# Kernel optimization log

Hardware: AMD Instinct MI355X
Metric: run time of the kernel (lower is better)

Reference implementation:

```python
import jax, jax.numpy as jnp
import numpy as np

EPS = 1e-06
H = 25  # num heads


def _rmsnorm(x, w, eps=EPS):
    # normalize over last dim in float32, as in the torch module
    xf = x.astype(jnp.float32)
    var = jnp.mean(xf * xf, axis=-1, keepdims=True)
    return (w * (xf * jax.lax.rsqrt(var + eps))).astype(x.dtype)


def setup_inputs() -> dict:
    key = jax.random.key(0)
    ks = jax.random.split(key, 4)
    B, N, C = 8, 1025, 3200
    x = jax.random.normal(ks[0], (B, N, C), dtype=jnp.float32)
    qkv_w = jax.random.normal(ks[1], (C, 3 * C), dtype=jnp.float32) * (C ** -0.5)
    qkv_b = jnp.zeros((3 * C,), dtype=jnp.float32)
    q_norm_w = jnp.ones((C,), dtype=jnp.float32)
    k_norm_w = jnp.ones((C,), dtype=jnp.float32)
    proj_w = jax.random.normal(ks[2], (C, C), dtype=jnp.float32) * (C ** -0.5)
    proj_b = jnp.zeros((C,), dtype=jnp.float32)
    return {"x": x, "qkv_w": qkv_w, "qkv_b": qkv_b, "q_norm_w": q_norm_w,
            "k_norm_w": k_norm_w, "proj_w": proj_w, "proj_b": proj_b}


def reference(x, qkv_w, qkv_b, q_norm_w, k_norm_w, proj_w, proj_b):
    B, N, C = x.shape
    D = C // H
    scale = D ** -0.5
    qkv = x @ qkv_w + qkv_b                      # [B, N, 3C]
    q, k, v = jnp.split(qkv, 3, axis=-1)         # each [B, N, C]
    # QK RMSNorm is over the FULL embed_dim (heads flattened), per source.
    q = _rmsnorm(q, q_norm_w)
    k = _rmsnorm(k, k_norm_w)
    q = q.reshape(B, N, H, D)
    k = k.reshape(B, N, H, D)
    v = v.reshape(B, N, H, D)
    attn = jnp.einsum('bqhd,bkhd->bhqk', q * scale, k)   # [B, H, N, N]
    attn = jax.nn.softmax(attn, axis=-1)
    out = jnp.einsum('bhqk,bkhd->bqhd', attn, v).reshape(B, N, C)
    return out @ proj_w + proj_b
```

## Files before the change

### kernel.cpp

```cpp
#include <hip/hip_runtime.h>
#include <hip/hip_bf16.h>
#include <math.h>

#define B_ 8
#define N_ 1025
#define C_ 3200
#define H_ 25
#define D_ 128
#define M_ (B_ * N_)
#define C3_ (3 * C_)

typedef unsigned short u16;
typedef unsigned int u32;
typedef short bf16x8 __attribute__((ext_vector_type(8)));
typedef float f32x4 __attribute__((ext_vector_type(4)));

__device__ inline void load_lds16(const void* g, void* s) {
    __builtin_amdgcn_global_load_lds(
        (const __attribute__((address_space(1))) void*)g,
        (__attribute__((address_space(3))) void*)s, 16, 0, 0);
}

__device__ inline void split_pair(float x0, float x1, u32& hpk, u32& lpk) {
    __hip_bfloat162 h2 = __float22bfloat162_rn(float2{x0, x1});
    union { __hip_bfloat162 b; u32 u; } cv; cv.b = h2;
    u32 h = cv.u;
    float hf0 = __uint_as_float(h << 16);
    float hf1 = __uint_as_float(h & 0xFFFF0000u);
    __hip_bfloat162 l2 = __float22bfloat162_rn(float2{x0 - hf0, x1 - hf1});
    union { __hip_bfloat162 b; u32 u; } cl; cl.b = l2;
    hpk = h; lpk = cl.u;
}

__device__ inline void split1(float x, u16& h, u16& l) {
    union { __hip_bfloat16 b; u16 u; } ch, cl;
    ch.b = __float2bfloat16(x);
    float hf = __uint_as_float(((u32)ch.u) << 16);
    cl.b = __float2bfloat16(x - hf);
    h = ch.u; l = cl.u;
}

__global__ __launch_bounds__(256) void convert_tsplit(
    const float* __restrict__ in, u16* __restrict__ hi, u16* __restrict__ lo,
    int K, int Nn, int strideN)
{
    __shared__ float T[32][33];
    const int tid = threadIdx.x;
    const int nb = blockIdx.x * 32, kb = blockIdx.y * 32;
    #pragma unroll
    for (int p = 0; p < 4; ++p) {
        int k = p * 8 + (tid >> 5), n = tid & 31;
        T[k][n] = in[(size_t)(kb + k) * strideN + nb + n];
    }
    __syncthreads();
    const int nn = tid >> 3, k0 = (tid & 7) * 4;
    u32 h0, l0, h1, l1;
    split_pair(T[k0][nn], T[k0 + 1][nn], h0, l0);
    split_pair(T[k0 + 2][nn], T[k0 + 3][nn], h1, l1);
    size_t o = (size_t)(nb + nn) * K + kb + k0;
    *(uint2*)&hi[o] = make_uint2(h0, h1);
    *(uint2*)&lo[o] = make_uint2(l0, l1);
}

__global__ __launch_bounds__(256) void gemm_asplit(
    const float* __restrict__ A,
    const u16* __restrict__ Bh, const u16* __restrict__ Bl,
    const float* __restrict__ bias, float* __restrict__ Cc,
    int M, int N, int ldc)
{
    __shared__ u16 As_h[4][128][8];
    __shared__ u16 As_l[4][128][8];
    __shared__ u16 Bs_h[4][128][8];
    __shared__ u16 Bs_l[4][128][8];

    const int tid  = threadIdx.x;
    const int lane = tid & 63;
    const int w    = tid >> 6;
    const int wm   = w & 1, wn = w >> 1;
    const int lr = lane & 15, lg = lane >> 4;

    const int gX   = gridDim.x;
    const int nwg  = gX * gridDim.y;
    const int orig = blockIdx.y * gX + blockIdx.x;
    const int q8 = nwg >> 3, r8 = nwg & 7;
    const int xcd = orig & 7, oi = orig >> 3;
    const int wg = (xcd < r8 ? xcd * (q8 + 1)
                             : r8 * (q8 + 1) + (xcd - r8) * q8) + oi;
    const int rowBase = (wg / gX) * 128;
    const int colBase = (wg % gX) * 128;

    const int arow = tid >> 1;
    const int akh  = (tid & 1) * 16;
    const int kc0  = akh >> 3;
    int gr0 = rowBase + arow; if (gr0 >= M) gr0 = M - 1;
    const float* aptr = A + (size_t)gr0 * C_ + akh;

    f32x4 acc[4][4] = {};

    float4 a0 = *(const float4*)(aptr + 0);
    float4 a1 = *(const float4*)(aptr + 4);
    float4 a2 = *(const float4*)(aptr + 8);
    float4 a3 = *(const float4*)(aptr + 12);

    for (int k0 = 0; k0 < C_; k0 += 32) {
        #pragma unroll
        for (int p = 0; p < 2; ++p) {
            int c = p * 256 + tid;
            int row = c & 127, kc = c >> 7;
            int ldsOff = (p * 256 + w * 64) * 8;
            size_t boff = (size_t)(colBase + row) * C_ + k0 + kc * 8;
            load_lds16(Bh + boff, (u16*)Bs_h + ldsOff);
            load_lds16(Bl + boff, (u16*)Bs_l + ldsOff);
        }
        u32 h0,h1,h2,h3,h4,h5,h6,h7, l0,l1,l2,l3,l4,l5,l6,l7;
        split_pair(a0.x, a0.y, h0, l0); split_pair(a0.z, a0.w, h1, l1);
        split_pair(a1.x, a1.y, h2, l2); split_pair(a1.z, a1.w, h3, l3);
        split_pair(a2.x, a2.y, h4, l4); split_pair(a2.z, a2.w, h5, l5);
        split_pair(a3.x, a3.y, h6, l6); split_pair(a3.z, a3.w, h7, l7);
        *(uint4*)&As_h[kc0][arow][0]     = make_uint4(h0, h1, h2, h3);
        *(uint4*)&As_h[kc0 + 1][arow][0] = make_uint4(h4, h5, h6, h7);
        *(uint4*)&As_l[kc0][arow][0]     = make_uint4(l0, l1, l2, l3);
        *(uint4*)&As_l[kc0 + 1][arow][0] = make_uint4(l4, l5, l6, l7);
        if (k0 + 32 < C_) {
            const float* ap = aptr + k0 + 32;
            a0 = *(const float4*)(ap + 0);
            a1 = *(const float4*)(ap + 4);
            a2 = *(const float4*)(ap + 8);
            a3 = *(const float4*)(ap + 12);
        }
        __syncthreads();

        bf16x8 ah[4], al[4], bh[4], bl[4];
        #pragma unroll
        for (int i = 0; i < 4; ++i) {
            ah[i] = *(const bf16x8*)&As_h[lg][wm * 64 + i * 16 + lr][0];
            al[i] = *(const bf16x8*)&As_l[lg][wm * 64 + i * 16 + lr][0];
            bh[i] = *(const bf16x8*)&Bs_h[lg][wn * 64 + i * 16 + lr][0];
            bl[i] = *(const bf16x8*)&Bs_l[lg][wn * 64 + i * 16 + lr][0];
        }
        #pragma unroll
        for (int j = 0; j < 4; ++j)
            #pragma unroll
            for (int i = 0; i < 4; ++i)
                acc[i][j] = __builtin_amdgcn_mfma_f32_16x16x32_bf16(
                    ah[i], bh[j], acc[i][j], 0, 0, 0);
        #pragma unroll
        for (int j = 0; j < 4; ++j)
            #pragma unroll
            for (int i = 0; i < 4; ++i)
                acc[i][j] = __builtin_amdgcn_mfma_f32_16x16x32_bf16(
                    al[i], bh[j], acc[i][j], 0, 0, 0);
        #pragma unroll
        for (int j = 0; j < 4; ++j)
            #pragma unroll
            for (int i = 0; i < 4; ++i)
                acc[i][j] = __builtin_amdgcn_mfma_f32_16x16x32_bf16(
                    ah[i], bl[j], acc[i][j], 0, 0, 0);
        __syncthreads();
    }

    #pragma unroll
    for (int i = 0; i < 4; ++i) {
        #pragma unroll
        for (int j = 0; j < 4; ++j) {
            int gc = colBase + wn * 64 + j * 16 + lr;
            float bv = bias[gc];
            #pragma unroll
            for (int r = 0; r < 4; ++r) {
                int gr = rowBase + wm * 64 + i * 16 + lg * 4 + r;
                if (gr < M) Cc[(size_t)gr * ldc + gc] = acc[i][j][r] + bv;
            }
        }
    }
}

__global__ __launch_bounds__(256) void gemm_bf16split(
    const u16* __restrict__ Ah, const u16* __restrict__ Al,
    const u16* __restrict__ Bh, const u16* __restrict__ Bl,
    const float* __restrict__ bias, float* __restrict__ Cc,
    int M, int N, int ldc)
{
    __shared__ u16 As_h[4][128][8];
    __shared__ u16 As_l[4][128][8];
    __shared__ u16 Bs_h[4][128][8];
    __shared__ u16 Bs_l[4][128][8];

    const int tid  = threadIdx.x;
    const int lane = tid & 63;
    const int w    = tid >> 6;
    const int wm   = w & 1, wn = w >> 1;
    const int lr = lane & 15, lg = lane >> 4;

    const int gX   = gridDim.x;
    const int nwg  = gX * gridDim.y;
    const int orig = blockIdx.y * gX + blockIdx.x;
    const int q8 = nwg >> 3, r8 = nwg & 7;
    const int xcd = orig & 7, oi = orig >> 3;
    const int wg = (xcd < r8 ? xcd * (q8 + 1)
                             : r8 * (q8 + 1) + (xcd - r8) * q8) + oi;
    const int rowBase = (wg / gX) * 128;
    const int colBase = (wg % gX) * 128;

    f32x4 acc[4][4] = {};

    for (int k0 = 0; k0 < C_; k0 += 32) {
        #pragma unroll
        for (int p = 0; p < 2; ++p) {
            int c = p * 256 + tid;
            int row = c & 127, kc = c >> 7;
            int ldsOff = (p * 256 + w * 64) * 8;
            int ar = rowBase + row; if (ar >= M) ar = M - 1;
            size_t aoff = (size_t)ar * C_ + k0 + kc * 8;
            size_t boff = (size_t)(colBase + row) * C_ + k0 + kc * 8;
            load_lds16(Ah + aoff, (u16*)As_h + ldsOff);
            load_lds16(Al + aoff, (u16*)As_l + ldsOff);
            load_lds16(Bh + boff, (u16*)Bs_h + ldsOff);
            load_lds16(Bl + boff, (u16*)Bs_l + ldsOff);
        }
        __syncthreads();

        bf16x8 ah[4], al[4], bh[4], bl[4];
        #pragma unroll
        for (int i = 0; i < 4; ++i) {
            ah[i] = *(const bf16x8*)&As_h[lg][wm * 64 + i * 16 + lr][0];
            al[i] = *(const bf16x8*)&As_l[lg][wm * 64 + i * 16 + lr][0];
            bh[i] = *(const bf16x8*)&Bs_h[lg][wn * 64 + i * 16 + lr][0];
            bl[i] = *(const bf16x8*)&Bs_l[lg][wn * 64 + i * 16 + lr][0];
        }
        #pragma unroll
        for (int j = 0; j < 4; ++j)
            #pragma unroll
            for (int i = 0; i < 4; ++i)
                acc[i][j] = __builtin_amdgcn_mfma_f32_16x16x32_bf16(
                    ah[i], bh[j], acc[i][j], 0, 0, 0);
        #pragma unroll
        for (int j = 0; j < 4; ++j)
            #pragma unroll
            for (int i = 0; i < 4; ++i)
                acc[i][j] = __builtin_amdgcn_mfma_f32_16x16x32_bf16(
                    al[i], bh[j], acc[i][j], 0, 0, 0);
        #pragma unroll
        for (int j = 0; j < 4; ++j)
            #pragma unroll
            for (int i = 0; i < 4; ++i)
                acc[i][j] = __builtin_amdgcn_mfma_f32_16x16x32_bf16(
                    ah[i], bl[j], acc[i][j], 0, 0, 0);
        __syncthreads();
    }

    #pragma unroll
    for (int i = 0; i < 4; ++i) {
        #pragma unroll
        for (int j = 0; j < 4; ++j) {
            int gc = colBase + wn * 64 + j * 16 + lr;
            float bv = bias[gc];
            #pragma unroll
            for (int r = 0; r < 4; ++r) {
                int gr = rowBase + wm * 64 + i * 16 + lg * 4 + r;
                if (gr < M) Cc[(size_t)gr * ldc + gc] = acc[i][j][r] + bv;
            }
        }
    }
}

__global__ __launch_bounds__(256) void rmsnorm_kernel(
    float* __restrict__ qkv, const float* __restrict__ qw,
    const float* __restrict__ kw)
{
    const int row   = blockIdx.x >> 1;
    const int which = blockIdx.x & 1;
    float* p = qkv + (size_t)row * C3_ + which * C_;
    const float* w = which ? kw : qw;
    const int tid = threadIdx.x;

    float ss = 0.f;
    for (int i = tid; i < C_ / 4; i += 256) {
        float4 v = ((const float4*)p)[i];
        ss += v.x * v.x + v.y * v.y + v.z * v.z + v.w * v.w;
    }
    #pragma unroll
    for (int off = 32; off; off >>= 1) ss += __shfl_down(ss, off);

    __shared__ float wsum[4];
    __shared__ float stot;
    if ((tid & 63) == 0) wsum[tid >> 6] = ss;
    __syncthreads();
    if (tid == 0) stot = wsum[0] + wsum[1] + wsum[2] + wsum[3];
    __syncthreads();

    const float scale = rsqrtf(stot / (float)C_ + 1e-6f);
    for (int i = tid; i < C_ / 4; i += 256) {
        float4 v  = ((const float4*)p)[i];
        float4 wv = ((const float4*)w)[i];
        v.x *= scale * wv.x; v.y *= scale * wv.y;
        v.z *= scale * wv.z; v.w *= scale * wv.w;
        ((float4*)p)[i] = v;
    }
}

__global__ __launch_bounds__(256, 2) void flash_mfma(
    const float* __restrict__ qkv, u16* __restrict__ aoh, u16* __restrict__ aol)
{
    __shared__ u16 Kh[4][32][32];
    __shared__ u16 Kl[4][32][32];
    __shared__ u16 Vth[128][40];
    __shared__ u16 Vtl[128][40];
    __shared__ u16 Ph[4][16][40];
    __shared__ u16 Pl[4][16][40];

    const int b   = blockIdx.z;
    const int h   = blockIdx.y;
    const int q0  = blockIdx.x * 64;
    const int tid = threadIdx.x;
    const int lane = tid & 63;
    const int w    = tid >> 6;
    const int lr = lane & 15, lg = lane >> 4;
    const float scale = 0.088388347648318447f;

    bf16x8 qh[4], ql[4];
    {
        int qr = q0 + w * 16 + lr;
        if (qr >= N_) qr = N_ - 1;
        const float* qp = qkv + (size_t)(b * N_ + qr) * C3_ + h * D_;
        #pragma unroll
        for (int c = 0; c < 4; ++c) {
            float4 x0 = *(const float4*)(qp + c * 32 + lg * 8);
            float4 x1 = *(const float4*)(qp + c * 32 + lg * 8 + 4);
            union { u32 u[4]; bf16x8 v; } Hq, Lq;
            split_pair(x0.x * scale, x0.y * scale, Hq.u[0], Lq.u[0]);
            split_pair(x0.z * scale, x0.w * scale, Hq.u[1], Lq.u[1]);
            split_pair(x1.x * scale, x1.y * scale, Hq.u[2], Lq.u[2]);
            split_pair(x1.z * scale, x1.w * scale, Hq.u[3], Lq.u[3]);
            qh[c] = Hq.v; ql[c] = Lq.v;
        }
    }

    const float* Kbase = qkv + (size_t)b * N_ * C3_ + C_ + h * D_;
    const float* Vbase = qkv + (size_t)b * N_ * C3_ + 2 * C_ + h * D_;

    const int skr = tid >> 3;
    const int skd = (tid & 7) * 16;
    const int svk = (tid & 15) * 2;
    const int svd = (tid >> 4) * 4;

    float4 kg[4], vg[2][2];

    auto stage_load = [&](int kt) {
        int kk = kt * 32 + skr;
        if (kk < N_) {
            const float* p = Kbase + (size_t)kk * C3_ + skd;
            kg[0] = *(const float4*)(p + 0);
            kg[1] = *(const float4*)(p + 4);
            kg[2] = *(const float4*)(p + 8);
            kg[3] = *(const float4*)(p + 12);
        } else {
            kg[0] = kg[1] = kg[2] = kg[3] = make_float4(0.f, 0.f, 0.f, 0.f);
        }
        #pragma unroll
        for (int r = 0; r < 2; ++r) {
            int vk = kt * 32 + svk + r;
            if (vk < N_) {
                const float* p = Vbase + (size_t)vk * C3_ + svd;
                vg[0][r] = *(const float4*)(p);
                vg[1][r] = *(const float4*)(p + 64);
            } else {
                vg[0][r] = make_float4(0.f, 0.f, 0.f, 0.f);
                vg[1][r] = make_float4(0.f, 0.f, 0.f, 0.f);
            }
        }
    };

    auto stage_store = [&]() {
        #pragma unroll
        for (int i = 0; i < 4; ++i) {
            int d = skd + i * 4;
            int c = d >> 5, dd = d & 31;
            u32 h0, l0, h1, l1;
            split_pair(kg[i].x, kg[i].y, h0, l0);
            split_pair(kg[i].z, kg[i].w, h1, l1);
            *(uint2*)&Kh[c][skr][dd] = make_uint2(h0, h1);
            *(uint2*)&Kl[c][skr][dd] = make_uint2(l0, l1);
        }
        #pragma unroll
        for (int half = 0; half < 2; ++half) {
            float a0[4] = { vg[half][0].x, vg[half][0].y, vg[half][0].z, vg[half][0].w };
            float a1[4] = { vg[half][1].x, vg[half][1].y, vg[half][1].z, vg[half][1].w };
            #pragma unroll
            for (int i = 0; i < 4; ++i) {
                int d = svd + half * 64 + i;
                u32 hp, lp;
                split_pair(a0[i], a1[i], hp, lp);
                *(u32*)&Vth[d][svk] = hp;
                *(u32*)&Vtl[d][svk] = lp;
            }
        }
    };

    f32x4 oacc[8] = {};
    float m[4]    = { -INFINITY, -INFINITY, -INFINITY, -INFINITY };
    float lsum[4] = { 0.f, 0.f, 0.f, 0.f };

    const int nkt = (N_ + 31) / 32;
    stage_load(0);
    for (int kt = 0; kt < nkt; ++kt) {
        __syncthreads();
        stage_store();
        __syncthreads();
        if (kt + 1 < nkt) stage_load(kt + 1);

        f32x4 s0 = {}, s1 = {};
        #pragma unroll
        for (int c = 0; c < 4; ++c) {
            bf16x8 kh0 = *(const bf16x8*)&Kh[c][lr][lg * 8];
            bf16x8 kl0 = *(const bf16x8*)&Kl[c][lr][lg * 8];
            bf16x8 kh1 = *(const bf16x8*)&Kh[c][16 + lr][lg * 8];
            bf16x8 kl1 = *(const bf16x8*)&Kl[c][16 + lr][lg * 8];
            s0 = __builtin_amdgcn_mfma_f32_16x16x32_bf16(qh[c], kh0, s0, 0, 0, 0);
            s0 = __builtin_amdgcn_mfma_f32_16x16x32_bf16(ql[c], kh0, s0, 0, 0, 0);
            s0 = __builtin_amdgcn_mfma_f32_16x16x32_bf16(qh[c], kl0, s0, 0, 0, 0);
            s1 = __builtin_amdgcn_mfma_f32_16x16x32_bf16(qh[c], kh1, s1, 0, 0, 0);
            s1 = __builtin_amdgcn_mfma_f32_16x16x32_bf16(ql[c], kh1, s1, 0, 0, 0);
            s1 = __builtin_amdgcn_mfma_f32_16x16x32_bf16(qh[c], kl1, s1, 0, 0, 0);
        }

        const int kb = kt * 32;
        const bool v0 = (kb + lr) < N_;
        const bool v1 = (kb + 16 + lr) < N_;
        #pragma unroll
        for (int r = 0; r < 4; ++r) {
            if (!v0) s0[r] = -INFINITY;
            if (!v1) s1[r] = -INFINITY;
        }

        #pragma unroll
        for (int r = 0; r < 4; ++r) {
            float mt = fmaxf(s0[r], s1[r]);
            mt = fmaxf(mt, __shfl_xor(mt, 1));
            mt = fmaxf(mt, __shfl_xor(mt, 2));
            mt = fmaxf(mt, __shfl_xor(mt, 4));
            mt = fmaxf(mt, __shfl_xor(mt, 8));
            float mn = fmaxf(m[r], mt);
            float al = __expf(m[r] - mn);
            m[r] = mn;
            float p0 = __expf(s0[r] - mn);
            float p1 = __expf(s1[r] - mn);
            float ls = p0 + p1;
            ls += __shfl_xor(ls, 1);
            ls += __shfl_xor(ls, 2);
            ls += __shfl_xor(ls, 4);
            ls += __shfl_xor(ls, 8);
            lsum[r] = lsum[r] * al + ls;
            #pragma unroll
            for (int dt = 0; dt < 8; ++dt) oacc[dt][r] *= al;

            u16 hh, ll;
            split1(p0, hh, ll);
            Ph[w][lg * 4 + r][lr] = hh;
            Pl[w][lg * 4 + r][lr] = ll;
            split1(p1, hh, ll);
            Ph[w][lg * 4 + r][16 + lr] = hh;
            Pl[w][lg * 4 + r][16 + lr] = ll;
        }

        bf16x8 pah = *(const bf16x8*)&Ph[w][lr][lg * 8];
        bf16x8 pal = *(const bf16x8*)&Pl[w][lr][lg * 8];
        #pragma unroll
        for (int dt = 0; dt < 8; ++dt) {
            bf16x8 vh = *(const bf16x8*)&Vth[dt * 16 + lr][lg * 8];
            bf16x8 vl = *(const bf16x8*)&Vtl[dt * 16 + lr][lg * 8];
            oacc[dt] = __builtin_amdgcn_mfma_f32_16x16x32_bf16(pah, vh, oacc[dt], 0, 0, 0);
            oacc[dt] = __builtin_amdgcn_mfma_f32_16x16x32_bf16(pal, vh, oacc[dt], 0, 0, 0);
            oacc[dt] = __builtin_amdgcn_mfma_f32_16x16x32_bf16(pah, vl, oacc[dt], 0, 0, 0);
        }
    }

    #pragma unroll
    for (int r = 0; r < 4; ++r) {
        int q = q0 + w * 16 + lg * 4 + r;
        if (q < N_) {
            float inv = 1.f / lsum[r];
            size_t base = (size_t)(b * N_ + q) * C_ + h * D_ + lr;
            #pragma unroll
            for (int dt = 0; dt < 8; ++dt) {
                u16 hh, ll;
                split1(oacc[dt][r] * inv, hh, ll);
                aoh[base + dt * 16] = hh;
                aol[base + dt * 16] = ll;
            }
        }
    }
}

extern "C" void kernel_launch(void* const* d_in, const int* in_sizes, int n_in,
                              void* d_out, int out_size, void* d_ws, size_t ws_size,
                              hipStream_t stream)
{
    const float* x        = (const float*)d_in[0];
    const float* qkv_w    = (const float*)d_in[1];
    const float* qkv_b    = (const float*)d_in[2];
    const float* q_norm_w = (const float*)d_in[3];
    const float* k_norm_w = (const float*)d_in[4];
    const float* proj_w   = (const float*)d_in[5];
    const float* proj_b   = (const float*)d_in[6];
    float* out = (float*)d_out;

    const size_t fQ = (size_t)M_ * C3_;
    const size_t fA = (size_t)M_ * C_;
    const size_t wC = (size_t)C_ * C_;

    float* qkv = (float*)d_ws;
    u16*   R   = (u16*)(qkv + fQ);

    dim3 blk(256);

    u16* wh = R;
    u16* wl = wh + wC;
    for (int j = 0; j < 3; ++j) {
        convert_tsplit<<<dim3(C_ / 32, C_ / 32), blk, 0, stream>>>(
            qkv_w + (size_t)j * C_, wh, wl, C_, C_, C3_);
        gemm_asplit<<<dim3(C_ / 128, (M_ + 127) / 128), blk, 0, stream>>>(
            x, wh, wl, qkv_b + j * C_, qkv + (size_t)j * C_, M_, C_, C3_);
    }

    rmsnorm_kernel<<<dim3(M_ * 2), blk, 0, stream>>>(qkv, q_norm_w, k_norm_w);
    u16* aoh = R;
    u16* aol = R + fA;
    flash_mfma<<<dim3((N_ + 63) / 64, H_, B_), blk, 0, stream>>>(qkv, aoh, aol);

    u16* ph = (u16*)d_ws;
    u16* pl = ph + wC;
    convert_tsplit<<<dim3(C_ / 32, C_ / 32), blk, 0, stream>>>(
        proj_w, ph, pl, C_, C_, C_);
    gemm_bf16split<<<dim3(C_ / 128, (M_ + 127) / 128), blk, 0, stream>>>(
        aoh, aol, ph, pl, proj_b, out, M_, C_, C_);
}
```

Baseline: 4.305 ms.

## Double-buffer LDS tiles in split-bf16 GEMMs to overlap loads with MFMA

Both split-bf16 GEMM kernels now keep two LDS tile buffers and issue the global-to-LDS loads for the next K step before computing on the current one. Partial vmcnt waits replace full __syncthreads. The aim is to hide global memory latency behind the MFMA work. In exchange, LDS use per block doubles, which may lower occupancy, and the hand-written waitcnt counts must match the number of loads in flight.

```diff
diff --git a/kernel.cpp b/kernel.cpp
--- a/kernel.cpp
+++ b/kernel.cpp
@@ -68,10 +68,10 @@
     const float* __restrict__ bias, float* __restrict__ Cc,
     int M, int N, int ldc)
 {
-    __shared__ u16 As_h[4][128][8];
-    __shared__ u16 As_l[4][128][8];
-    __shared__ u16 Bs_h[4][128][8];
-    __shared__ u16 Bs_l[4][128][8];
+    __shared__ u16 As_h[2][512][8];
+    __shared__ u16 As_l[2][512][8];
+    __shared__ u16 Bs_h[2][512][8];
+    __shared__ u16 Bs_l[2][512][8];
 
     const int tid  = threadIdx.x;
     const int lane = tid & 63;
@@ -89,54 +89,88 @@
     const int rowBase = (wg / gX) * 128;
     const int colBase = (wg % gX) * 128;
 
+    const int brow = tid & 127, bkc = tid >> 7;
+    const size_t boff0 = (size_t)(colBase + brow) * C_ + bkc * 8;
+    const size_t boff1 = (size_t)(colBase + brow) * C_ + (bkc + 2) * 8;
+    const int ldsA = (w * 64) * 8;
+    const int ldsB = (256 + w * 64) * 8;
+
     const int arow = tid >> 1;
     const int akh  = (tid & 1) * 16;
     const int kc0  = akh >> 3;
     int gr0 = rowBase + arow; if (gr0 >= M) gr0 = M - 1;
     const float* aptr = A + (size_t)gr0 * C_ + akh;
 
+    auto STAGE_B = [&](int bb, int k0) {
+        const int bo = bb * 512 * 8;
+        load_lds16(Bh + boff0 + k0, (u16*)Bs_h + bo + ldsA);
+        load_lds16(Bl + boff0 + k0, (u16*)Bs_l + bo + ldsA);
+        load_lds16(Bh + boff1 + k0, (u16*)Bs_h + bo + ldsB);
+        load_lds16(Bl + boff1 + k0, (u16*)Bs_l + bo + ldsB);
+    };
+
+    auto ASPLIT = [&](int bb, const float4& x0, const float4& x1,
+                      const float4& x2, const float4& x3) {
+        u32 h0,h1,h2,h3,h4,h5,h6,h7, l0,l1,l2,l3,l4,l5,l6,l7;
+        split_pair(x0.x, x0.y, h0, l0); split_pair(x0.z, x0.w, h1, l1);
+        split_pair(x1.x, x1.y, h2, l2); split_pair(x1.z, x1.w, h3, l3);
+        split_pair(x2.x, x2.y, h4, l4); split_pair(x2.z, x2.w, h5, l5);
+        split_pair(x3.x, x3.y, h6, l6); split_pair(x3.z, x3.w, h7, l7);
+        *(uint4*)&As_h[bb][kc0 * 128 + arow][0]       = make_uint4(h0,h1,h2,h3);
+        *(uint4*)&As_h[bb][(kc0 + 1) * 128 + arow][0] = make_uint4(h4,h5,h6,h7);
+        *(uint4*)&As_l[bb][kc0 * 128 + arow][0]       = make_uint4(l0,l1,l2,l3);
+        *(uint4*)&As_l[bb][(kc0 + 1) * 128 + arow][0] = make_uint4(l4,l5,l6,l7);
+    };
+
     f32x4 acc[4][4] = {};
-
-    float4 a0 = *(const float4*)(aptr + 0);
-    float4 a1 = *(const float4*)(aptr + 4);
-    float4 a2 = *(const float4*)(aptr + 8);
-    float4 a3 = *(const float4*)(aptr + 12);
-
+    float4 a0, a1, a2, a3;
+
+    {
+        float4 p0 = *(const float4*)(aptr + 0);
+        float4 p1 = *(const float4*)(aptr + 4);
+        float4 p2 = *(const float4*)(aptr + 8);
+        float4 p3 = *(const float4*)(aptr + 12);
+        ASPLIT(0, p0, p1, p2, p3);
+    }
+    STAGE_B(0, 0);
+    {
+        const float* ap = aptr + 32;
+        a0 = *(const float4*)(ap + 0);
+        a1 = *(const float4*)(ap + 4);
+        a2 = *(const float4*)(ap + 8);
+        a3 = *(const float4*)(ap + 12);
+    }
+    asm volatile("s_waitcnt vmcnt(0) lgkmcnt(0)" ::: "memory");
+    __builtin_amdgcn_s_barrier();
+    asm volatile("" ::: "memory");
+
+    int cur = 0;
     for (int k0 = 0; k0 < C_; k0 += 32) {
-        #pragma unroll
-        for (int p = 0; p < 2; ++p) {
-            int c = p * 256 + tid;
-            int row = c & 127, kc = c >> 7;
-            int ldsOff = (p * 256 + w * 64) * 8;
-            size_t boff = (size_t)(colBase + row) * C_ + k0 + kc * 8;
-            load_lds16(Bh + boff, (u16*)Bs_h + ldsOff);
-            load_lds16(Bl + boff, (u16*)Bs_l + ldsOff);
-        }
-        u32 h0,h1,h2,h3,h4,h5,h6,h7, l0,l1,l2,l3,l4,l5,l6,l7;
-        split_pair(a0.x, a0.y, h0, l0); split_pair(a0.z, a0.w, h1, l1);
-        split_pair(a1.x, a1.y, h2, l2); split_pair(a1.z, a1.w, h3, l3);
-        split_pair(a2.x, a2.y, h4, l4); split_pair(a2.z, a2.w, h5, l5);
-        split_pair(a3.x, a3.y, h6, l6); split_pair(a3.z, a3.w, h7, l7);
-        *(uint4*)&As_h[kc0][arow][0]     = make_uint4(h0, h1, h2, h3);
-        *(uint4*)&As_h[kc0 + 1][arow][0] = make_uint4(h4, h5, h6, h7);
-        *(uint4*)&As_l[kc0][arow][0]     = make_uint4(l0, l1, l2, l3);
-        *(uint4*)&As_l[kc0 + 1][arow][0] = make_uint4(l4, l5, l6, l7);
         if (k0 + 32 < C_) {
-            const float* ap = aptr + k0 + 32;
-            a0 = *(const float4*)(ap + 0);
-            a1 = *(const float4*)(ap + 4);
-            a2 = *(const float4*)(ap + 8);
-            a3 = *(const float4*)(ap + 12);
-        }
-        __syncthreads();
+            STAGE_B(cur ^ 1, k0 + 32);
+            ASPLIT(cur ^ 1, a0, a1, a2, a3);
+            if (k0 + 64 < C_) {
+                const float* ap = aptr + k0 + 64;
+                a0 = *(const float4*)(ap + 0);
+                a1 = *(const float4*)(ap + 4);
+                a2 = *(const float4*)(ap + 8);
+                a3 = *(const float4*)(ap + 12);
+            }
+            asm volatile("s_waitcnt vmcnt(8)" ::: "memory");
+        } else {
+            asm volatile("s_waitcnt vmcnt(0)" ::: "memory");
+        }
+        asm volatile("s_waitcnt lgkmcnt(0)" ::: "memory");
+        __builtin_amdgcn_s_barrier();
+        asm volatile("" ::: "memory");
 
         bf16x8 ah[4], al[4], bh[4], bl[4];
         #pragma unroll
         for (int i = 0; i < 4; ++i) {
-            ah[i] = *(const bf16x8*)&As_h[lg][wm * 64 + i * 16 + lr][0];
-            al[i] = *(const bf16x8*)&As_l[lg][wm * 64 + i * 16 + lr][0];
-            bh[i] = *(const bf16x8*)&Bs_h[lg][wn * 64 + i * 16 + lr][0];
-            bl[i] = *(const bf16x8*)&Bs_l[lg][wn * 64 + i * 16 + lr][0];
+            ah[i] = *(const bf16x8*)&As_h[cur][lg * 128 + wm * 64 + i * 16 + lr][0];
+            al[i] = *(const bf16x8*)&As_l[cur][lg * 128 + wm * 64 + i * 16 + lr][0];
+            bh[i] = *(const bf16x8*)&Bs_h[cur][lg * 128 + wn * 64 + i * 16 + lr][0];
+            bl[i] = *(const bf16x8*)&Bs_l[cur][lg * 128 + wn * 64 + i * 16 + lr][0];
         }
         #pragma unroll
         for (int j = 0; j < 4; ++j)
@@ -156,7 +190,11 @@
             for (int i = 0; i < 4; ++i)
                 acc[i][j] = __builtin_amdgcn_mfma_f32_16x16x32_bf16(
                     ah[i], bl[j], acc[i][j], 0, 0, 0);
-        __syncthreads();
+
+        asm volatile("s_waitcnt lgkmcnt(0)" ::: "memory");
+        __builtin_amdgcn_s_barrier();
+        asm volatile("" ::: "memory");
+        cur ^= 1;
     }
 
     #pragma unroll
@@ -180,10 +218,10 @@
     const float* __restrict__ bias, float* __restrict__ Cc,
     int M, int N, int ldc)
 {
-    __shared__ u16 As_h[4][128][8];
-    __shared__ u16 As_l[4][128][8];
-    __shared__ u16 Bs_h[4][128][8];
-    __shared__ u16 Bs_l[4][128][8];
+    __shared__ u16 As_h[2][512][8];
+    __shared__ u16 As_l[2][512][8];
+    __shared__ u16 Bs_h[2][512][8];
+    __shared__ u16 Bs_l[2][512][8];
 
     const int tid  = threadIdx.x;
     const int lane = tid & 63;
@@ -201,31 +239,48 @@
     const int rowBase = (wg / gX) * 128;
     const int colBase = (wg % gX) * 128;
 
+    const int row = tid & 127, kc = tid >> 7;
+    int ar = rowBase + row; if (ar >= M) ar = M - 1;
+    const size_t aoff0 = (size_t)ar * C_ + kc * 8;
+    const size_t aoff1 = (size_t)ar * C_ + (kc + 2) * 8;
+    const size_t boff0 = (size_t)(colBase + row) * C_ + kc * 8;
+    const size_t boff1 = (size_t)(colBase + row) * C_ + (kc + 2) * 8;
+    const int ldsA = (w * 64) * 8;
+    const int ldsB = (256 + w * 64) * 8;
+
+    auto STAGE = [&](int bb, int k0) {
+        const int bo = bb * 512 * 8;
+        load_lds16(Ah + aoff0 + k0, (u16*)As_h + bo + ldsA);
+        load_lds16(Al + aoff0 + k0, (u16*)As_l + bo + ldsA);
+        load_lds16(Bh + boff0 + k0, (u16*)Bs_h + bo + ldsA);
+        load_lds16(Bl + boff0 + k0, (u16*)Bs_l + bo + ldsA);
+        load_lds16(Ah + aoff1 + k0, (u16*)As_h + bo + ldsB);
+        load_lds16(Al + aoff1 + k0, (u16*)As_l + bo + ldsB);
+        load_lds16(Bh + boff1 + k0, (u16*)Bs_h + bo + ldsB);
+        load_lds16(Bl + boff1 + k0, (u16*)Bs_l + bo + ldsB);
+    };
+
     f32x4 acc[4][4] = {};
 
+    STAGE(0, 0);
+    int cur = 0;
     for (int k0 = 0; k0 < C_; k0 += 32) {
-        #pragma unroll
-        for (int p = 0; p < 2; ++p) {
-            int c = p * 256 + tid;
-            int row = c & 127, kc = c >> 7;
-            int ldsOff = (p * 256 + w * 64) * 8;
-            int ar = rowBase + row; if (ar >= M) ar = M - 1;
-            size_t aoff = (size_t)ar * C_ + k0 + kc * 8;
-            size_t boff = (size_t)(colBase + row) * C_ + k0 + kc * 8;
-            load_lds16(Ah + aoff, (u16*)As_h + ldsOff);
-            load_lds16(Al + aoff, (u16*)As_l + ldsOff);
-            load_lds16(Bh + boff, (u16*)Bs_h + ldsOff);
-            load_lds16(Bl + boff, (u16*)Bs_l + ldsOff);
-        }
-        __syncthreads();
+        if (k0 + 32 < C_) {
+            STAGE(cur ^ 1, k0 + 32);
+            asm volatile("s_waitcnt vmcnt(8)" ::: "memory");
+        } else {
+            asm volatile("s_waitcnt vmcnt(0)" ::: "memory");
+        }
+        __builtin_amdgcn_s_barrier();
+        asm volatile("" ::: "memory");
 
         bf16x8 ah[4], al[4], bh[4], bl[4];
         #pragma unroll
         for (int i = 0; i < 4; ++i) {
-            ah[i] = *(const bf16x8*)&As_h[lg][wm * 64 + i * 16 + lr][0];
-            al[i] = *(const bf16x8*)&As_l[lg][wm * 64 + i * 16 + lr][0];
-            bh[i] = *(const bf16x8*)&Bs_h[lg][wn * 64 + i * 16 + lr][0];
-            bl[i] = *(const bf16x8*)&Bs_l[lg][wn * 64 + i * 16 + lr][0];
+            ah[i] = *(const bf16x8*)&As_h[cur][lg * 128 + wm * 64 + i * 16 + lr][0];
+            al[i] = *(const bf16x8*)&As_l[cur][lg * 128 + wm * 64 + i * 16 + lr][0];
+            bh[i] = *(const bf16x8*)&Bs_h[cur][lg * 128 + wn * 64 + i * 16 + lr][0];
+            bl[i] = *(const bf16x8*)&Bs_l[cur][lg * 128 + wn * 64 + i * 16 + lr][0];
         }
         #pragma unroll
         for (int j = 0; j < 4; ++j)
@@ -245,7 +300,11 @@
             for (int i = 0; i < 4; ++i)
                 acc[i][j] = __builtin_amdgcn_mfma_f32_16x16x32_bf16(
                     ah[i], bl[j], acc[i][j], 0, 0, 0);
-        __syncthreads();
+
+        asm volatile("s_waitcnt lgkmcnt(0)" ::: "memory");
+        __builtin_amdgcn_s_barrier();
+        asm volatile("" ::: "memory");
+        cur ^= 1;
     }
 
     #pragma unroll
```

After: 4.507 ms. 4.7% more time.
